# Optimization experiments

Hardware: AMD Instinct MI355X
Metric: run time of the kernel (lower is better)

## Reference

```python
import jax, jax.numpy as jnp
import numpy as np

GRID = (128, 128, 128)
CENTER = np.array([0.0, 0.0, 0.0], dtype=np.float32)
SIZE = np.array([214.0, 214.0, 214.0], dtype=np.float32)
N_LORS = 65536
_CRYSTAL = SIZE[2] / GRID[2]
KERNEL_WIDTH = float(np.sqrt(_CRYSTAL * _CRYSTAL / np.pi))  # TOR gaussian sigma


def _make_lors(key, n, s):
    # rows: x1, y1, z1, x2, y2, z2 ; main direction along the 3rd coordinate
    k1, k2 = jax.random.split(key)
    trans = jax.random.uniform(k1, (4, n), jnp.float32, -0.45 * s, 0.45 * s)
    jit = jax.random.uniform(k2, (2, n), jnp.float32, -0.02 * s, 0.02 * s)
    half = 0.5 * s
    return jnp.stack([trans[0], trans[1], -half + jit[0],
                      trans[2], trans[3], half + jit[1]]).astype(jnp.float32)


def _project_bp(lors, image, grid, center, size, sigma):
    """TOR (tube-of-response) projection + listmode backprojection.
    lors: [N,6]; image shape == grid; main ray axis = last grid axis.
    Returns (line_integrals [N], backprojection volume grid)."""
    n0, n1, n2 = grid
    center = jnp.asarray(center, jnp.float32)
    size = jnp.asarray(size, jnp.float32)
    vox = size / jnp.array(grid, jnp.float32)
    xmin = center[0] - 0.5 * size[0]
    ymin = center[1] - 0.5 * size[1]
    zmin = center[2] - 0.5 * size[2]
    p1, p2 = lors[:, 0:3], lors[:, 3:6]
    d = p2 - p1
    L = jnp.sqrt(jnp.sum(d * d, axis=1))                    # [N]
    dz = d[:, 2]
    dz = jnp.where(jnp.abs(dz) < 1e-6, 1e-6, dz)
    zc = zmin + (jnp.arange(n2, dtype=jnp.float32) + 0.5) * vox[2]  # [K]
    t = (zc[None, :] - p1[:, 2:3]) / dz[:, None]            # [N,K] ray param per slice
    xs = p1[:, 0:1] + t * d[:, 0:1]                         # [N,K]
    ys = p1[:, 1:2] + t * d[:, 1:2]
    fi = (xs - xmin) / vox[0] - 0.5
    fj = (ys - ymin) / vox[1] - 0.5
    i0 = jnp.round(fi).astype(jnp.int32)
    j0 = jnp.round(fj).astype(jnp.int32)
    off = jnp.arange(-1, 2, dtype=jnp.int32)                # 3x3 in-plane TOR window
    oi = jnp.repeat(off, 3)                                  # [9]
    oj = jnp.tile(off, 3)                                    # [9]
    ii = i0[..., None] + oi                                  # [N,K,9]
    jj = j0[..., None] + oj
    inb = ((ii >= 0) & (ii < n0) & (jj >= 0) & (jj < n1)
           & (t[..., None] >= 0.0) & (t[..., None] <= 1.0))
    iic = jnp.clip(ii, 0, n0 - 1)
    jjc = jnp.clip(jj, 0, n1 - 1)
    dxv = (xmin + (iic.astype(jnp.float32) + 0.5) * vox[0]) - xs[..., None]
    dyv = (ymin + (jjc.astype(jnp.float32) + 0.5) * vox[1]) - ys[..., None]
    w = jnp.exp(-(dxv * dxv + dyv * dyv) / (2.0 * sigma * sigma))
    w = jnp.where(inb, w, 0.0)                               # [N,K,9]
    dl = vox[2] * L / jnp.abs(dz)                            # path length per slice [N]
    kk = jnp.broadcast_to(jnp.arange(n2, dtype=jnp.int32)[None, :, None], ii.shape)
    vals = image[iic, jjc, kk]                               # gather [N,K,9]
    proj = jnp.sum(w * vals, axis=(1, 2)) * dl               # [N]
    # listmode MLEM backprojection of 1/projection along same TOR weights
    contrib = w * (dl / (proj + 1e-8))[:, None, None]        # [N,K,9]
    flat = (iic * n1 + jjc) * n2 + kk
    bp = jnp.zeros(n0 * n1 * n2, jnp.float32).at[flat.reshape(-1)].add(
        contrib.reshape(-1)).reshape(n0, n1, n2)
    return proj, bp


def setup_inputs() -> dict:
    key = jax.random.key(0)
    kimg, keff, kx, ky, kz = jax.random.split(key, 5)
    image = jax.random.uniform(kimg, GRID, jnp.float32, 0.5, 1.5)
    effmap = jax.random.uniform(keff, GRID, jnp.float32, 0.5, 1.5)
    s = float(SIZE[0])
    return {
        'image': image,
        'efficiency_map': effmap,
        'xlors': _make_lors(kx, N_LORS, s),
        'ylors': _make_lors(ky, N_LORS, s),
        'zlors': _make_lors(kz, N_LORS, s),
    }


def reference(image, efficiency_map, xlors, ylors, zlors):
    g0, g1, g2 = GRID
    sigma = KERNEL_WIDTH
    imgz = image
    imgx = jnp.transpose(imgz, (2, 0, 1))
    imgy = jnp.transpose(imgz, (1, 0, 2))
    # stored as [6, N] -> [N, 6]
    xl, yl, zl = xlors.T, ylors.T, zlors.T
    pz, bpz = _project_bp(zl, imgz, GRID, CENTER, SIZE, sigma)
    gridx = (g0, g2, g1)
    px, bpx = _project_bp(xl, imgx, gridx, CENTER[[0, 2, 1]], SIZE[[0, 2, 1]], sigma)
    bpxt = jnp.transpose(bpx, (1, 2, 0))
    gridy = (g1, g2, g0)
    py, bpy = _project_bp(yl, imgy, gridy, CENTER[[1, 2, 0]], SIZE[[1, 2, 0]], sigma)
    bpyt = jnp.transpose(bpy, (1, 0, 2))
    return imgz / (efficiency_map + 1e-8) * (bpxt + bpyt + bpz)
```

## Files before the change

kernel.cpp:

```cpp
#include <hip/hip_runtime.h>
#include <hip/hip_fp16.h>
#include <math.h>

#define NLOR  65536
#define NG    128
#define PLANE (NG * NG)
#define NSUB  2
#define KG    8
#define NKG   (NG / KG)

#define VOX    1.671875f
#define XMIN  (-107.0f)
#define C2     1.57079632679f

#define FPSCALE    8388608.0f
#define INVFPSCALE (1.0f / 8388608.0f)

#define PRM_STRIDE 8

template<int SP, int SQ, int SR, int CONTIG, int NSUM, bool ACCUM, bool FINAL>
__device__ __forceinline__ void permute_body(
    const float* __restrict__ in, float* __restrict__ out,
    const float* __restrict__ img, const float* __restrict__ eff,
    int b, float (*tile)[33])
{
    const int c0 = blockIdx.x * 32;
    const int r0 = blockIdx.y * 32;
    const int tx = threadIdx.x, ty = threadIdx.y;

#pragma unroll
    for (int m = 0; m < 4; ++m) {
        const int C = c0 + tx;
        const int R = r0 + ty + 8 * m;
        const int P = (CONTIG == 0) ? C : b;
        const int Q = (CONTIG == 0) ? b : C;
        const int a = P * SP + Q * SQ + R * SR;
        float v = 0.0f;
#pragma unroll
        for (int s = 0; s < NSUM; ++s) v += in[a + s * NG * PLANE];
        tile[ty + 8 * m][tx] = v;
    }
    __syncthreads();
#pragma unroll
    for (int m = 0; m < 4; ++m) {
        const int R = r0 + tx;
        const int C = c0 + ty + 8 * m;
        const int P = (CONTIG == 0) ? C : b;
        const int Q = (CONTIG == 0) ? b : C;
        const int o = P * PLANE + Q * NG + R;
        float v = tile[tx][ty + 8 * m];
        if (ACCUM) v += out[o];
        if (FINAL) v = img[o] / (eff[o] + 1e-8f) * v;
        out[o] = v;
    }
}

template<int SP, int SQ, int SR, int CONTIG>
__device__ __forceinline__ void permute_half_body(
    const float* __restrict__ in, __half* __restrict__ out,
    int b, float (*tile)[33])
{
    const int c0 = blockIdx.x * 32;
    const int r0 = blockIdx.y * 32;
    const int tx = threadIdx.x, ty = threadIdx.y;

#pragma unroll
    for (int m = 0; m < 4; ++m) {
        const int C = c0 + tx;
        const int R = r0 + ty + 8 * m;
        const int P = (CONTIG == 0) ? C : b;
        const int Q = (CONTIG == 0) ? b : C;
        tile[ty + 8 * m][tx] = in[P * SP + Q * SQ + R * SR];
    }
    __syncthreads();
#pragma unroll
    for (int m = 0; m < 4; ++m) {
        const int R = r0 + tx;
        const int C = c0 + ty + 8 * m;
        const int P = (CONTIG == 0) ? C : b;
        const int Q = (CONTIG == 0) ? b : C;
        const int o = P * PLANE + Q * NG + R;
        out[o] = __float2half(tile[tx][ty + 8 * m]);
    }
}

__global__ __launch_bounds__(256)
void perm_img2(const float* __restrict__ image,
               __half* __restrict__ imgPz, __half* __restrict__ imgPx)
{
    __shared__ float tile[32][33];
    const int b = blockIdx.z;
    if (b < 128)
        permute_half_body<1, 16384, 128, 0>(image, imgPz, b, tile);
    else
        permute_half_body<128, 1, 16384, 1>(image, imgPx, b - 128, tile);
}

__global__ __launch_bounds__(256)
void perm_outA(const float* __restrict__ in, float* __restrict__ out)
{
    __shared__ float tile[32][33];
    permute_body<128, 1, 16384, 1, NSUB, false, false>(in, out, nullptr, nullptr, blockIdx.z, tile);
}

__global__ __launch_bounds__(256)
void perm_outB(const float* __restrict__ in, float* __restrict__ out,
               const float* __restrict__ img, const float* __restrict__ eff)
{
    __shared__ float tile[32][33];
    permute_body<1, 16384, 128, 0, NSUB, true, true>(in, out, img, eff, blockIdx.z, tile);
}

__global__ __launch_bounds__(256)
void lor_prep(const float* __restrict__ zl, const float* __restrict__ yl,
              const float* __restrict__ xl,
              float* __restrict__ prmz, float* __restrict__ prmy,
              float* __restrict__ prmx)
{
    const int f = blockIdx.y;
    const float* lors = (f == 0) ? zl : (f == 1) ? yl : xl;
    float* prm        = (f == 0) ? prmz : (f == 1) ? prmy : prmx;
    const int lor = blockIdx.x * 256 + threadIdx.x;

    const float p1x = lors[0 * NLOR + lor];
    const float p1y = lors[1 * NLOR + lor];
    const float p1z = lors[2 * NLOR + lor];
    const float dx  = lors[3 * NLOR + lor] - p1x;
    const float dy  = lors[4 * NLOR + lor] - p1y;
    float dz = lors[5 * NLOR + lor] - p1z;
    dz = (fabsf(dz) < 1e-6f) ? 1e-6f : dz;
    const float rdz = 1.0f / dz;

    const float t0 = (XMIN + 0.5f * VOX - p1z) * rdz;
    const float dt = VOX * rdz;
    float u0 = (fmaf(t0, dx, p1x) - XMIN) * (1.0f / VOX) - 0.5f;
    float v0 = (fmaf(t0, dy, p1y) - XMIN) * (1.0f / VOX) - 0.5f;
    float du = dx * rdz;
    float dv = dy * rdz;
    if (f == 1) {
        float tmp = u0; u0 = v0; v0 = tmp;
        tmp = du; du = dv; dv = tmp;
    }
    float4* p4 = (float4*)(prm + (size_t)lor * PRM_STRIDE);
    p4[0] = make_float4(u0, du, v0, dv);
    p4[1] = make_float4(t0, dt, 0.0f, 0.0f);
}

template<int NS>
__device__ __forceinline__ void proj_body(
    const float* const* prmv, const unsigned int* __restrict__ imgP,
    float* const* p8v, unsigned int* pl)
{
    const int g     = blockIdx.x;
    const int chunk = blockIdx.y;
    const int tid   = threadIdx.x;
    const int lor0  = chunk * 2048 + tid;
    const float k0  = (float)(g * KG);

    float tA[2 * NS], uA[2 * NS], vA[2 * NS], dtA[2 * NS], duA[2 * NS], dvA[2 * NS], sA[2 * NS];
#pragma unroll
    for (int s = 0; s < 2 * NS; ++s) {
        const float* prm = prmv[s >> 1];
        const int lor = lor0 + (s & 1) * 1024;
        const float4* p4 = (const float4*)(prm + (size_t)lor * PRM_STRIDE);
        const float4 a = p4[0];
        const float4 b = p4[1];
        tA[s] = fmaf(k0, b.y, b.x);  dtA[s] = b.y;
        uA[s] = fmaf(k0, a.y, a.x);  duA[s] = a.y;
        vA[s] = fmaf(k0, a.w, a.z);  dvA[s] = a.w;
        sA[s] = 0.0f;
    }

    for (int st = 0; st < KG; ++st) {
        const int k = g * KG + st;
        const uint4* src = (const uint4*)(imgP + k * (NG * 64));
        uint4* dst = (uint4*)pl;
        for (int i = tid; i < (NG * 64) / 4; i += 1024) dst[i] = src[i];
        __syncthreads();

        const float fst = (float)st;
#pragma unroll
        for (int s = 0; s < 2 * NS; ++s) {
            const float t = fmaf(fst, dtA[s], tA[s]);
            const float u = fmaf(fst, duA[s], uA[s]);
            const float v = fmaf(fst, dvA[s], vA[s]);
            const int i0 = (int)rintf(u);
            const int j0 = (int)rintf(v);
            const float mi = (float)i0 - u;
            const float mj = (float)j0 - v;
            const float mim = mi - 1.0f, mip = mi + 1.0f;
            const float mjm = mj - 1.0f, mjp = mj + 1.0f;
            const float exm = __expf(-C2 * mim * mim);
            const float ex0 = __expf(-C2 * mi  * mi );
            const float exq = __expf(-C2 * mip * mip);
            const float eym = __expf(-C2 * mjm * mjm);
            const float ey0 = __expf(-C2 * mj  * mj );
            const float eyq = __expf(-C2 * mjp * mjp);

            const int odd = j0 & 1;
            const float lA = odd ? eym : 0.0f;
            const float hA = odd ? ey0 : eym;
            const float lB = odd ? eyq : ey0;
            const float hB = odd ? 0.0f : eyq;
            const int p0 = min(max((j0 - 1) >> 1, 0), 62);
            const int ib = min(max(i0 - 1, 0), 125);

            const float exv[3] = {exm, ex0, exq};
            float acc = 0.0f;
#pragma unroll
            for (int a = 0; a < 3; ++a) {
                const int rowb = (ib + a) << 6;
                const unsigned int Aw = pl[rowb + p0];
                const unsigned int Bw = pl[rowb + p0 + 1];
                const float2 A = __half22float2(*reinterpret_cast<const __half2*>(&Aw));
                const float2 B = __half22float2(*reinterpret_cast<const __half2*>(&Bw));
                acc += exv[a] * (lA * A.x + hA * A.y + lB * B.x + hB * B.y);
            }
            const bool tin = (t >= 0.0f) && (t <= 1.0f);
            sA[s] += tin ? acc : 0.0f;
        }
        __syncthreads();
    }
#pragma unroll
    for (int s = 0; s < NS; ++s) {
        p8v[s][g * NLOR + lor0]        = sA[2 * s];
        p8v[s][g * NLOR + lor0 + 1024] = sA[2 * s + 1];
    }
}

__global__ __launch_bounds__(1024, 8)
void proj_all(const float* __restrict__ prmz, const float* __restrict__ prmy,
              const float* __restrict__ prmx,
              const unsigned int* __restrict__ imgPz, const unsigned int* __restrict__ imgPx,
              float* __restrict__ p8z, float* __restrict__ p8y,
              float* __restrict__ p8x)
{
    __shared__ unsigned int pl[NG * 64];
    if (blockIdx.z == 0) {
        const float* prmv[2] = {prmz, prmy};
        float* p8v[2] = {p8z, p8y};
        proj_body<2>(prmv, imgPz, p8v, pl);
    } else {
        const float* prmv[1] = {prmx};
        float* p8v[1] = {p8x};
        proj_body<1>(prmv, imgPx, p8v, pl);
    }
}

__global__ __launch_bounds__(256)
void reduce_cf3(const float* __restrict__ zl, const float* __restrict__ yl,
                const float* __restrict__ xl,
                const float* __restrict__ p8z, const float* __restrict__ p8y,
                const float* __restrict__ p8x,
                float* __restrict__ prmz, float* __restrict__ prmy,
                float* __restrict__ prmx)
{
    const int which = blockIdx.y;
    const float* lors  = (which == 0) ? zl  : (which == 1) ? yl  : xl;
    const float* part8 = (which == 0) ? p8z : (which == 1) ? p8y : p8x;
    float*       prm   = (which == 0) ? prmz : (which == 1) ? prmy : prmx;

    const int lor = blockIdx.x * 256 + threadIdx.x;
    float s = 0.0f;
#pragma unroll
    for (int g = 0; g < NKG; ++g) s += part8[g * NLOR + lor];

    const float p1x = lors[0 * NLOR + lor];
    const float p1y = lors[1 * NLOR + lor];
    const float p1z = lors[2 * NLOR + lor];
    const float dx  = lors[3 * NLOR + lor] - p1x;
    const float dy  = lors[4 * NLOR + lor] - p1y;
    const float dz0 = lors[5 * NLOR + lor] - p1z;
    const float L = sqrtf(dx * dx + dy * dy + dz0 * dz0);
    const float adz = fmaxf(fabsf(dz0), 1e-6f);
    const float dl = VOX * L / adz;
    prm[(size_t)lor * PRM_STRIDE + 6] = dl / (s * dl + 1e-8f);
}

__device__ __forceinline__ void bp_deposit(const float* __restrict__ prm,
    int lor, float fk, unsigned int* __restrict__ pl)
{
    const float4* p4 = (const float4*)(prm + (size_t)lor * PRM_STRIDE);
    const float4 a = p4[0];
    const float4 b = p4[1];
    const float t = fmaf(fk, b.y, b.x);
    const float u = fmaf(fk, a.y, a.x);
    const float v = fmaf(fk, a.w, a.z);
    const bool tin = (t >= 0.0f) && (t <= 1.0f);
    if (!tin) return;

    const float fi = rintf(u);
    const float fj = rintf(v);
    const int i0 = (int)fi;
    const int j0 = (int)fj;
    const float cfs = b.z * FPSCALE;

    const float mi = fi - u;
    const float mj = fj - v;
    const float mim = mi - 1.0f, mip = mi + 1.0f;
    const float mjm = mj - 1.0f, mjp = mj + 1.0f;
    const float exm = __expf(-C2 * mim * mim) * cfs;
    const float ex0 = __expf(-C2 * mi  * mi ) * cfs;
    const float exq = __expf(-C2 * mip * mip) * cfs;
    const float eym = __expf(-C2 * mjm * mjm);
    const float ey0 = __expf(-C2 * mj  * mj );
    const float eyq = __expf(-C2 * mjp * mjp);

    const int ib = min(max(i0 - 1, 0), NG - 3);
    const int jb = min(max(j0 - 1, 0), NG - 3);
    unsigned int* base = pl + ib * NG + jb;

    const float exv[3] = {exm, ex0, exq};
#pragma unroll
    for (int aa = 0; aa < 3; ++aa) {
        unsigned int* row = base + aa * NG;
        atomicAdd(row + 0, (unsigned int)(exv[aa] * eym));
        atomicAdd(row + 1, (unsigned int)(exv[aa] * ey0));
        atomicAdd(row + 2, (unsigned int)(exv[aa] * eyq));
    }
}

__global__ __launch_bounds__(1024)
void bp_all(const float* __restrict__ prmz, const float* __restrict__ prmy,
            const float* __restrict__ prmx,
            float* __restrict__ bpsubA, float* __restrict__ bpsubB)
{
    __shared__ unsigned int pl[NG * NG];
    const int k   = blockIdx.x >> 1;
    const int sub = blockIdx.x & 1;
    const int tid = threadIdx.x;

    for (int i = tid; i < NG * NG; i += 1024) pl[i] = 0u;
    __syncthreads();

    const float fk = (float)k;
    const int lo = sub * (NLOR / NSUB), hi = lo + NLOR / NSUB;
    float* bpsub;
    if (blockIdx.y == 0) {
        for (int lor = lo + tid; lor < hi; lor += 1024)
            bp_deposit(prmz, lor, fk, pl);
        for (int lor = lo + tid; lor < hi; lor += 1024)
            bp_deposit(prmy, lor, fk, pl);
        bpsub = bpsubA;
    } else {
        for (int lor = lo + tid; lor < hi; lor += 1024)
            bp_deposit(prmx, lor, fk, pl);
        bpsub = bpsubB;
    }
    __syncthreads();

    float4* out4 = (float4*)(bpsub + ((size_t)sub * NG + k) * PLANE);
    const uint4* pl4 = (const uint4*)pl;
    for (int i = tid; i < (NG * NG) / 4; i += 1024) {
        const uint4 vv = pl4[i];
        out4[i] = make_float4((float)vv.x * INVFPSCALE, (float)vv.y * INVFPSCALE,
                              (float)vv.z * INVFPSCALE, (float)vv.w * INVFPSCALE);
    }
}

extern "C" void kernel_launch(void* const* d_in, const int* in_sizes, int n_in,
                              void* d_out, int out_size, void* d_ws, size_t ws_size,
                              hipStream_t stream) {
    const float* image = (const float*)d_in[0];
    const float* eff   = (const float*)d_in[1];
    const float* xl    = (const float*)d_in[2];
    const float* yl    = (const float*)d_in[3];
    const float* zl    = (const float*)d_in[4];
    float* out = (float*)d_out;

    char* ws = (char*)d_ws;
    __half* imgPz = (__half*)(ws);
    __half* imgPx = (__half*)(ws + (size_t)( 4 << 20));
    float* bpsubA = (float*)(ws + (size_t)( 8 << 20));
    float* bpsubB = (float*)(ws + (size_t)(24 << 20));
    float* p8z    = (float*)(ws + (size_t)(40 << 20));
    float* p8y    = (float*)(ws + (size_t)(44 << 20));
    float* p8x    = (float*)(ws + (size_t)(48 << 20));
    float* prmz   = (float*)(ws + (size_t)(52 << 20));
    float* prmy   = (float*)(ws + (size_t)(54 << 20));
    float* prmx   = (float*)(ws + (size_t)(56 << 20));

    const dim3 tb(32, 8);

    lor_prep<<<dim3(NLOR / 256, 3), 256, 0, stream>>>(zl, yl, xl, prmz, prmy, prmx);
    perm_img2<<<dim3(4, 4, 256), tb, 0, stream>>>(image, imgPz, imgPx);
    proj_all<<<dim3(16, 32, 2), 1024, 0, stream>>>(prmz, prmy, prmx,
        (const unsigned int*)imgPz, (const unsigned int*)imgPx, p8z, p8y, p8x);
    reduce_cf3<<<dim3(256, 3), 256, 0, stream>>>(zl, yl, xl, p8z, p8y, p8x, prmz, prmy, prmx);
    bp_all<<<dim3(128 * NSUB, 2), 1024, 0, stream>>>(prmz, prmy, prmx, bpsubA, bpsubB);
    perm_outA<<<dim3(4, 4, 128), tb, 0, stream>>>(bpsubA, out);
    perm_outB<<<dim3(4, 4, 128), tb, 0, stream>>>(bpsubB, out, image, eff);
}
```

Before: 234.4 us.

## Fuse LOR prep into image permute, transpose in bp LDS, merge output permutes

Folds the LOR parameter setup into the image-permute kernel as extra z-blocks, which removes one launch. The backprojection plane in shared memory now uses a padded stride of 129, and the store transposes out of LDS, so partial volumes for one family come out already in output layout. The two output permute kernels become a single finalize kernel that reads the other family directly and applies the image/efficiency scaling. The deposit loops are unrolled and interleave the z and y families. This trades one fewer launch and one fewer full-volume read-modify-write for strided LDS reads during the bp writeout.

```diff
diff --git a/kernel.cpp b/kernel.cpp
--- a/kernel.cpp
+++ b/kernel.cpp
@@ -16,44 +16,9 @@
 #define FPSCALE    8388608.0f
 #define INVFPSCALE (1.0f / 8388608.0f)
 
+#define PLP    129
+
 #define PRM_STRIDE 8
-
-template<int SP, int SQ, int SR, int CONTIG, int NSUM, bool ACCUM, bool FINAL>
-__device__ __forceinline__ void permute_body(
-    const float* __restrict__ in, float* __restrict__ out,
-    const float* __restrict__ img, const float* __restrict__ eff,
-    int b, float (*tile)[33])
-{
-    const int c0 = blockIdx.x * 32;
-    const int r0 = blockIdx.y * 32;
-    const int tx = threadIdx.x, ty = threadIdx.y;
-
-#pragma unroll
-    for (int m = 0; m < 4; ++m) {
-        const int C = c0 + tx;
-        const int R = r0 + ty + 8 * m;
-        const int P = (CONTIG == 0) ? C : b;
-        const int Q = (CONTIG == 0) ? b : C;
-        const int a = P * SP + Q * SQ + R * SR;
-        float v = 0.0f;
-#pragma unroll
-        for (int s = 0; s < NSUM; ++s) v += in[a + s * NG * PLANE];
-        tile[ty + 8 * m][tx] = v;
-    }
-    __syncthreads();
-#pragma unroll
-    for (int m = 0; m < 4; ++m) {
-        const int R = r0 + tx;
-        const int C = c0 + ty + 8 * m;
-        const int P = (CONTIG == 0) ? C : b;
-        const int Q = (CONTIG == 0) ? b : C;
-        const int o = P * PLANE + Q * NG + R;
-        float v = tile[tx][ty + 8 * m];
-        if (ACCUM) v += out[o];
-        if (FINAL) v = img[o] / (eff[o] + 1e-8f) * v;
-        out[o] = v;
-    }
-}
 
 template<int SP, int SQ, int SR, int CONTIG>
 __device__ __forceinline__ void permute_half_body(
@@ -86,41 +51,28 @@
 
 __global__ __launch_bounds__(256)
 void perm_img2(const float* __restrict__ image,
-               __half* __restrict__ imgPz, __half* __restrict__ imgPx)
+               __half* __restrict__ imgPz, __half* __restrict__ imgPx,
+               const float* __restrict__ zl, const float* __restrict__ yl,
+               const float* __restrict__ xl,
+               float* __restrict__ prmz, float* __restrict__ prmy,
+               float* __restrict__ prmx)
 {
     __shared__ float tile[32][33];
     const int b = blockIdx.z;
-    if (b < 128)
+    if (b < 128) {
         permute_half_body<1, 16384, 128, 0>(image, imgPz, b, tile);
-    else
+        return;
+    }
+    if (b < 256) {
         permute_half_body<128, 1, 16384, 1>(image, imgPx, b - 128, tile);
-}
-
-__global__ __launch_bounds__(256)
-void perm_outA(const float* __restrict__ in, float* __restrict__ out)
-{
-    __shared__ float tile[32][33];
-    permute_body<128, 1, 16384, 1, NSUB, false, false>(in, out, nullptr, nullptr, blockIdx.z, tile);
-}
-
-__global__ __launch_bounds__(256)
-void perm_outB(const float* __restrict__ in, float* __restrict__ out,
-               const float* __restrict__ img, const float* __restrict__ eff)
-{
-    __shared__ float tile[32][33];
-    permute_body<1, 16384, 128, 0, NSUB, true, true>(in, out, img, eff, blockIdx.z, tile);
-}
-
-__global__ __launch_bounds__(256)
-void lor_prep(const float* __restrict__ zl, const float* __restrict__ yl,
-              const float* __restrict__ xl,
-              float* __restrict__ prmz, float* __restrict__ prmy,
-              float* __restrict__ prmx)
-{
-    const int f = blockIdx.y;
+        return;
+    }
+    const int linear = (b - 256) * 16 + blockIdx.y * 4 + blockIdx.x;
+    const int gid = linear * 256 + threadIdx.y * 32 + threadIdx.x;
+    const int f   = gid >> 16;
+    const int lor = gid & (NLOR - 1);
     const float* lors = (f == 0) ? zl : (f == 1) ? yl : xl;
     float* prm        = (f == 0) ? prmz : (f == 1) ? prmy : prmx;
-    const int lor = blockIdx.x * 256 + threadIdx.x;
 
     const float p1x = lors[0 * NLOR + lor];
     const float p1y = lors[1 * NLOR + lor];
@@ -308,12 +260,12 @@
 
     const int ib = min(max(i0 - 1, 0), NG - 3);
     const int jb = min(max(j0 - 1, 0), NG - 3);
-    unsigned int* base = pl + ib * NG + jb;
+    unsigned int* base = pl + ib * PLP + jb;
 
     const float exv[3] = {exm, ex0, exq};
 #pragma unroll
     for (int aa = 0; aa < 3; ++aa) {
-        unsigned int* row = base + aa * NG;
+        unsigned int* row = base + aa * PLP;
         atomicAdd(row + 0, (unsigned int)(exv[aa] * eym));
         atomicAdd(row + 1, (unsigned int)(exv[aa] * ey0));
         atomicAdd(row + 2, (unsigned int)(exv[aa] * eyq));
@@ -323,38 +275,67 @@
 __global__ __launch_bounds__(1024)
 void bp_all(const float* __restrict__ prmz, const float* __restrict__ prmy,
             const float* __restrict__ prmx,
-            float* __restrict__ bpsubA, float* __restrict__ bpsubB)
-{
-    __shared__ unsigned int pl[NG * NG];
+            float* __restrict__ bpA, float* __restrict__ bpB)
+{
+    __shared__ unsigned int pl[NG * PLP];
     const int k   = blockIdx.x >> 1;
     const int sub = blockIdx.x & 1;
     const int tid = threadIdx.x;
 
-    for (int i = tid; i < NG * NG; i += 1024) pl[i] = 0u;
+    for (int i = tid; i < NG * PLP; i += 1024) pl[i] = 0u;
     __syncthreads();
 
     const float fk = (float)k;
-    const int lo = sub * (NLOR / NSUB), hi = lo + NLOR / NSUB;
+    const int lo = sub * (NLOR / NSUB);
+    constexpr int NIT = (NLOR / NSUB) / 1024;
     float* bpsub;
     if (blockIdx.y == 0) {
-        for (int lor = lo + tid; lor < hi; lor += 1024)
+#pragma unroll 2
+        for (int it = 0; it < NIT; ++it) {
+            const int lor = lo + tid + it * 1024;
             bp_deposit(prmz, lor, fk, pl);
-        for (int lor = lo + tid; lor < hi; lor += 1024)
             bp_deposit(prmy, lor, fk, pl);
-        bpsub = bpsubA;
+        }
+        bpsub = bpA;
     } else {
-        for (int lor = lo + tid; lor < hi; lor += 1024)
-            bp_deposit(prmx, lor, fk, pl);
-        bpsub = bpsubB;
+#pragma unroll 4
+        for (int it = 0; it < NIT; ++it)
+            bp_deposit(prmx, lo + tid + it * 1024, fk, pl);
+        bpsub = bpB;
     }
     __syncthreads();
 
-    float4* out4 = (float4*)(bpsub + ((size_t)sub * NG + k) * PLANE);
-    const uint4* pl4 = (const uint4*)pl;
-    for (int i = tid; i < (NG * NG) / 4; i += 1024) {
-        const uint4 vv = pl4[i];
-        out4[i] = make_float4((float)vv.x * INVFPSCALE, (float)vv.y * INVFPSCALE,
-                              (float)vv.z * INVFPSCALE, (float)vv.w * INVFPSCALE);
+    float* dst = bpsub + ((size_t)(sub * NG + k)) * PLANE;
+    for (int idx = tid; idx < PLANE; idx += 1024)
+        dst[idx] = (float)pl[(idx & 127) * PLP + (idx >> 7)] * INVFPSCALE;
+}
+
+__global__ __launch_bounds__(256)
+void finalize_out(const float* __restrict__ bpA, const float* __restrict__ bpB,
+                  const float* __restrict__ img, const float* __restrict__ eff,
+                  float* __restrict__ out)
+{
+    __shared__ float tA[32][33];
+    const int b  = blockIdx.z;
+    const int x0 = blockIdx.x * 32;
+    const int z0 = blockIdx.y * 32;
+    const int tx = threadIdx.x, ty = threadIdx.y;
+    const int VOL = NG * PLANE;
+
+#pragma unroll
+    for (int m = 0; m < 4; ++m) {
+        const int z = z0 + ty + 8 * m;
+        const int a = z * PLANE + b * NG + (x0 + tx);
+        tA[ty + 8 * m][tx] = bpA[a] + bpA[a + VOL];
+    }
+    __syncthreads();
+#pragma unroll
+    for (int m = 0; m < 4; ++m) {
+        const int x  = x0 + ty + 8 * m;
+        const int o  = x * PLANE + b * NG + (z0 + tx);
+        const int bb = b * PLANE + x * NG + (z0 + tx);
+        const float v = tA[tx][ty + 8 * m] + bpB[bb] + bpB[bb + VOL];
+        out[o] = img[o] / (eff[o] + 1e-8f) * v;
     }
 }
 
@@ -371,8 +352,8 @@
     char* ws = (char*)d_ws;
     __half* imgPz = (__half*)(ws);
     __half* imgPx = (__half*)(ws + (size_t)( 4 << 20));
-    float* bpsubA = (float*)(ws + (size_t)( 8 << 20));
-    float* bpsubB = (float*)(ws + (size_t)(24 << 20));
+    float* bpA    = (float*)(ws + (size_t)( 8 << 20));
+    float* bpB    = (float*)(ws + (size_t)(24 << 20));
     float* p8z    = (float*)(ws + (size_t)(40 << 20));
     float* p8y    = (float*)(ws + (size_t)(44 << 20));
     float* p8x    = (float*)(ws + (size_t)(48 << 20));
@@ -382,12 +363,11 @@
 
     const dim3 tb(32, 8);
 
-    lor_prep<<<dim3(NLOR / 256, 3), 256, 0, stream>>>(zl, yl, xl, prmz, prmy, prmx);
-    perm_img2<<<dim3(4, 4, 256), tb, 0, stream>>>(image, imgPz, imgPx);
+    perm_img2<<<dim3(4, 4, 304), tb, 0, stream>>>(image, imgPz, imgPx,
+        zl, yl, xl, prmz, prmy, prmx);
     proj_all<<<dim3(16, 32, 2), 1024, 0, stream>>>(prmz, prmy, prmx,
         (const unsigned int*)imgPz, (const unsigned int*)imgPx, p8z, p8y, p8x);
     reduce_cf3<<<dim3(256, 3), 256, 0, stream>>>(zl, yl, xl, p8z, p8y, p8x, prmz, prmy, prmx);
-    bp_all<<<dim3(128 * NSUB, 2), 1024, 0, stream>>>(prmz, prmy, prmx, bpsubA, bpsubB);
-    perm_outA<<<dim3(4, 4, 128), tb, 0, stream>>>(bpsubA, out);
-    perm_outB<<<dim3(4, 4, 128), tb, 0, stream>>>(bpsubB, out, image, eff);
-}
+    bp_all<<<dim3(128 * NSUB, 2), 1024, 0, stream>>>(prmz, prmy, prmx, bpA, bpB);
+    finalize_out<<<dim3(4, 4, 128), tb, 0, stream>>>(bpA, bpB, image, eff, out);
+}
```

Result: faster. 226.7 us (-3.3%).
